# Kernel optimization log

Measured on AMD Instinct MI355X. Metric: run time of the kernel, lower is better.

Reference implementation:

```python
import jax, jax.numpy as jnp
import numpy as np
import math

N = 50000      # nodes
E = 600000     # edges
IN = 128       # in_channels
OUT = 128      # out_channels (heads * per-head)
H = 2          # heads
D = OUT // H   # per-head dim = 64
TDIM = 64      # time encoder out_channels
MSG = 64       # msg_dim
EDGE = TDIM + MSG  # edge_dim = 128


def setup_inputs() -> dict:
    key = jax.random.key(0)
    ks = jax.random.split(key, 16)
    s_in = 1.0 / math.sqrt(IN)
    s_ed = 1.0 / math.sqrt(EDGE)
    return {
        "x": jax.random.normal(ks[0], (N, IN), dtype=jnp.float32),
        "last_update": jax.random.randint(ks[1], (N,), 0, 1000000, dtype=jnp.int32),
        "edge_index": jax.random.randint(ks[2], (2, E), 0, N, dtype=jnp.int64),
        "t": jax.random.randint(ks[3], (E,), 0, 1000000, dtype=jnp.int32),
        "msg": jax.random.normal(ks[4], (E, MSG), dtype=jnp.float32),
        # TimeEncoder: cos(Linear(1 -> TDIM))
        "time_w": jax.random.normal(ks[5], (TDIM,), dtype=jnp.float32) * 0.01,
        "time_b": jax.random.normal(ks[6], (TDIM,), dtype=jnp.float32),
        # TransformerConv params (heads=2, per-head D, edge_dim=EDGE)
        "Wq": jax.random.normal(ks[7], (IN, H * D), dtype=jnp.float32) * s_in,
        "bq": jnp.zeros((H * D,), dtype=jnp.float32),
        "Wk": jax.random.normal(ks[8], (IN, H * D), dtype=jnp.float32) * s_in,
        "bk": jnp.zeros((H * D,), dtype=jnp.float32),
        "Wv": jax.random.normal(ks[9], (IN, H * D), dtype=jnp.float32) * s_in,
        "bv": jnp.zeros((H * D,), dtype=jnp.float32),
        "We": jax.random.normal(ks[10], (EDGE, H * D), dtype=jnp.float32) * s_ed,  # lin_edge, no bias
        "Wskip": jax.random.normal(ks[11], (IN, H * D), dtype=jnp.float32) * s_in,
        "bskip": jnp.zeros((H * D,), dtype=jnp.float32),
    }


def reference(x, last_update, edge_index, t, msg,
              time_w, time_b, Wq, bq, Wk, bk, Wv, bv, We, Wskip, bskip):
    src = edge_index[0]
    dst = edge_index[1]

    # rel_t = last_update[src] - t ; time encoding cos(w * rel_t + b)
    rel_t = (last_update[src] - t).astype(x.dtype)                 # [E]
    rel_t_enc = jnp.cos(rel_t[:, None] * time_w + time_b)          # [E, TDIM]
    edge_attr = jnp.concatenate([rel_t_enc, msg], axis=-1)         # [E, EDGE]

    n = x.shape[0]
    # Node projections, then per-edge gather (PyG: i = dst, j = src)
    q = (x @ Wq + bq).reshape(n, H, D)[dst]                        # [E, H, D]
    k = (x @ Wk + bk).reshape(n, H, D)[src]                        # [E, H, D]
    v = (x @ Wv + bv).reshape(n, H, D)[src]                        # [E, H, D]
    e = (edge_attr @ We).reshape(-1, H, D)                         # [E, H, D]

    k = k + e
    alpha = jnp.sum(q * k, axis=-1) / math.sqrt(D)                 # [E, H]

    # segment softmax over edges sharing the same destination node
    amax = jax.ops.segment_max(alpha, dst, num_segments=n)         # [N, H]
    ex = jnp.exp(alpha - amax[dst])                                # [E, H]
    denom = jax.ops.segment_sum(ex, dst, num_segments=n)           # [N, H]
    attn = ex / (denom[dst] + 1e-16)                               # [E, H]

    out_e = (v + e) * attn[..., None]                              # [E, H, D]
    out = jax.ops.segment_sum(out_e, dst, num_segments=n)          # [N, H, D]
    out = out.reshape(n, H * D)

    # root/skip connection (root_weight=True, beta=False)
    return out + (x @ Wskip + bskip)
```

## Files before the change

### kernel.cpp

```cpp
#include <hip/hip_runtime.h>
#include <hip/hip_bf16.h>

typedef __hip_bfloat16 bf16;
typedef __attribute__((ext_vector_type(8))) short bfrag;
typedef __attribute__((ext_vector_type(4))) float ffrag;

#define CDIM 128
#define TDIMC 64
#define MSGD 64
#define INV2PI 0.15915494309189535f
#define WCONV_BLOCKS 320

__device__ __forceinline__ unsigned short f2bf(float f) {
    union { __hip_bfloat16 h; unsigned short u; } cv;
    cv.h = __float2bfloat16(f);
    return cv.u;
}

__device__ __forceinline__ float fcos_rev(float xr) {
    float fr, c;
    asm("v_fract_f32 %0, %1" : "=v"(fr) : "v"(xr));
    asm("v_cos_f32 %0, %1" : "=v"(c) : "v"(fr));
    return c;
}

__global__ __launch_bounds__(256)
void prep_kernel(const int* __restrict__ ei, int E, int* __restrict__ count,
                 const float* __restrict__ Wq, const float* __restrict__ Wk,
                 const float* __restrict__ Wv, const float* __restrict__ Ws,
                 const float* __restrict__ We,
                 short* __restrict__ Wt, short* __restrict__ Wet) {
    int b = blockIdx.x;
    if (b < WCONV_BLOCKS) {
        int idx = b * 256 + threadIdx.x;
        if (idx >= 5 * 16384) return;
        int mat = idx >> 14;
        int r = idx & 16383;
        int n = r >> 7, kk = r & 127;
        const float* W = (mat == 0) ? Wq : (mat == 1) ? Wk : (mat == 2) ? Wv : (mat == 3) ? Ws : We;
        short bv = (short)f2bf(W[kk * 128 + n]);
        if (mat < 4) Wt[(size_t)mat * 16384 + n * 128 + kk] = bv;
        else         Wet[n * 128 + kk] = bv;
    } else {
        int e = (b - WCONV_BLOCKS) * 256 + threadIdx.x;
        int probe = (e < E) ? ei[2 * e + 1] : 0;
        int is32 = (__ballot(probe != 0) != 0ULL);
        if (e < E) {
            int d = is32 ? ei[E + e] : ei[2 * (E + e)];
            atomicAdd(&count[d], 1);
        }
    }
}

__global__ __launch_bounds__(1024)
void scan1_kernel(const int* __restrict__ count, int N,
                  int* __restrict__ cur, int* __restrict__ bsum) {
    __shared__ int wsum[16];
    __shared__ int woff[16];
    int t = threadIdx.x;
    int lane = t & 63, wv = t >> 6;
    int i = blockIdx.x * 1024 + t;
    int v = (i < N) ? count[i] : 0;
    int incl = v;
#pragma unroll
    for (int off = 1; off < 64; off <<= 1) {
        int n = __shfl_up(incl, off, 64);
        if (lane >= off) incl += n;
    }
    if (lane == 63) wsum[wv] = incl;
    __syncthreads();
    if (wv == 0) {
        int ws = (lane < 16) ? wsum[lane] : 0;
        int wi = ws;
#pragma unroll
        for (int off = 1; off < 16; off <<= 1) {
            int n = __shfl_up(wi, off, 64);
            if (lane >= off) wi += n;
        }
        if (lane < 16) woff[lane] = wi - ws;
        if (lane == 15) bsum[blockIdx.x] = wi;
    }
    __syncthreads();
    if (i < N) cur[i] = woff[wv] + incl - v;
}

__global__ void scan2_kernel(int* __restrict__ bsum, int nb) {
    int lane = threadIdx.x;
    int carry = 0;
    for (int base = 0; base < nb; base += 64) {
        int i = base + lane;
        int v = (i < nb) ? bsum[i] : 0;
        int incl = v;
#pragma unroll
        for (int off = 1; off < 64; off <<= 1) {
            int n = __shfl_up(incl, off, 64);
            if (lane >= off) incl += n;
        }
        if (i < nb) bsum[i] = carry + incl - v;
        carry += __shfl(incl, 63, 64);
    }
}

__global__ __launch_bounds__(256)
void sp_kernel(const float* __restrict__ x, const short* __restrict__ Wt,
               const float* __restrict__ bq, const float* __restrict__ bk,
               const float* __restrict__ bv, const float* __restrict__ bs,
               float* __restrict__ q, short* __restrict__ kvs,
               float* __restrict__ out, int N, int PB,
               const int* __restrict__ ei, int E,
               const int* __restrict__ tarr, const int* __restrict__ last_update,
               int* __restrict__ cur, const int* __restrict__ bsum,
               int4* __restrict__ ed_s) {
    __shared__ __attribute__((aligned(16))) short sx[64][136];
    int tid = threadIdx.x;
    if (blockIdx.x >= PB) {
        int e = (blockIdx.x - PB) * 256 + tid;
        int probe = (e < E) ? ei[2 * e + 1] : 0;
        int is32 = (__ballot(probe != 0) != 0ULL);
        if (e >= E) return;
        int s = is32 ? ei[e] : ei[2 * e];
        int d = is32 ? ei[E + e] : ei[2 * (E + e)];
        int pos = atomicAdd(&cur[d], 1) + bsum[d >> 10];
        float rt = (float)(last_update[s] - tarr[e]);
        ed_s[pos] = make_int4(s, d, e, __float_as_int(rt));
        return;
    }
    int n0 = blockIdx.x * 64;
    const float4* x4 = (const float4*)x;
    for (int i = tid; i < 64 * 32; i += 256) {
        int nl = i >> 5, c4 = i & 31;
        int n = n0 + nl;
        float4 f = (n < N) ? x4[(size_t)n * 32 + c4] : make_float4(0.f, 0.f, 0.f, 0.f);
        unsigned int lo = ((unsigned int)f2bf(f.y) << 16) | f2bf(f.x);
        unsigned int hi = ((unsigned int)f2bf(f.w) << 16) | f2bf(f.z);
        *(uint2*)&sx[nl][c4 * 4] = make_uint2(lo, hi);
    }
    __syncthreads();

    int lane = tid & 63, wv = tid >> 6;
    int n15 = lane & 15, quad = lane >> 4;
    const short* W = Wt + (size_t)wv * 16384;
    const float* bias = (wv == 0) ? bq : (wv == 1) ? bk : (wv == 2) ? bv : bs;

    ffrag acc[4][8];
#pragma unroll
    for (int r = 0; r < 4; ++r)
#pragma unroll
        for (int c = 0; c < 8; ++c)
            acc[r][c] = (ffrag){0.f, 0.f, 0.f, 0.f};

#pragma unroll
    for (int kc = 0; kc < 4; ++kc) {
        int kk = kc * 32 + quad * 8;
        bfrag a[4];
#pragma unroll
        for (int r = 0; r < 4; ++r)
            a[r] = *(const bfrag*)&sx[r * 16 + n15][kk];
#pragma unroll
        for (int c = 0; c < 8; ++c) {
            bfrag b = *(const bfrag*)&W[(c * 16 + n15) * 128 + kk];
#pragma unroll
            for (int r = 0; r < 4; ++r)
                acc[r][c] = __builtin_amdgcn_mfma_f32_16x16x32_bf16(a[r], b, acc[r][c], 0, 0, 0);
        }
    }

    if (wv == 1 || wv == 2) {
        int isv = (wv == 2) ? 2 : 0;
#pragma unroll
        for (int c = 0; c < 8; ++c) {
            int col = c * 16 + n15;
            float bval = bias[col];
            int coff = (col >> 1) * 4 + (col & 1) + isv;
#pragma unroll
            for (int r = 0; r < 4; ++r) {
#pragma unroll
                for (int g = 0; g < 4; ++g) {
                    int n = n0 + r * 16 + quad * 4 + g;
                    if (n < N) kvs[(size_t)n * 256 + coff] = (short)f2bf(acc[r][c][g] + bval);
                }
            }
        }
    } else {
        float* dstp = (wv == 0) ? q : out;
#pragma unroll
        for (int c = 0; c < 8; ++c) {
            int col = c * 16 + n15;
            float bval = bias[col];
#pragma unroll
            for (int r = 0; r < 4; ++r) {
#pragma unroll
                for (int g = 0; g < 4; ++g) {
                    int n = n0 + r * 16 + quad * 4 + g;
                    if (n < N) dstp[(size_t)n * CDIM + col] = acc[r][c][g] + bval;
                }
            }
        }
    }
}

#define LOADQ(KVA, QA, JB) do {                                                 \
    _Pragma("unroll")                                                           \
    for (int u = 0; u < 4; ++u) {                                               \
        int el = wv * 16 + (JB) * 4 + u;                                        \
        int s = s_src[el], d = s_dst[el];                                       \
        KVA[u] = kv[(size_t)s * 64 + lane];                                     \
        QA[u] = *(const float2*)&q[(size_t)d * CDIM + 2 * lane];                \
    } } while (0)

#define PROC(KVA, QA, JB) do {                                                  \
    _Pragma("unroll")                                                           \
    for (int u = 0; u < 4; ++u) {                                               \
        int el = wv * 16 + (JB) * 4 + u;                                        \
        unsigned int ep = *(const unsigned int*)&sbuf[el][2 * lane];            \
        float ex0 = __uint_as_float(ep << 16);                                  \
        float ex1 = __uint_as_float(ep & 0xffff0000u);                          \
        float kx = __uint_as_float(KVA[u].x << 16) + ex0;                       \
        float ky = __uint_as_float(KVA[u].x & 0xffff0000u) + ex1;               \
        float p = QA[u].x * kx + QA[u].y * ky;                                  \
        _Pragma("unroll")                                                       \
        for (int off = 1; off < 32; off <<= 1) p += __shfl_xor(p, off, 32);     \
        float exv = (e0 + el < E) ? __expf(p * 0.125f) : 0.f;                   \
        int d = s_dst[el];                                                      \
        if (d != cur_d) {                              \
            float* np = &num[(size_t)cur_d * CDIM + 2 * lane];                  \
            unsafeAtomicAdd(np, accx);                                          \
            unsafeAtomicAdd(np + 1, accy);                                      \
            if ((lane & 31) == 0) unsafeAtomicAdd(&den[cur_d * 2 + h], dacc);   \
            accx = 0.f; accy = 0.f; dacc = 0.f;                                 \
            cur_d = d;                                                          \
        }                                                                       \
        float vx = __uint_as_float(KVA[u].y << 16) + ex0;                       \
        float vy = __uint_as_float(KVA[u].y & 0xffff0000u) + ex1;               \
        accx = fmaf(vx, exv, accx);                                             \
        accy = fmaf(vy, exv, accy);                                             \
        dacc += exv;                                                            \
    } } while (0)

__global__ __launch_bounds__(256)
void edge_kernel(const int4* __restrict__ ed_s,
                 const float* __restrict__ msg,
                 const float* __restrict__ time_w, const float* __restrict__ time_b,
                 const short* __restrict__ Wet,
                 const float* __restrict__ q, const uint2* __restrict__ kv,
                 float* __restrict__ num, float* __restrict__ den,
                 int E) {
    __shared__ __attribute__((aligned(16))) short sbuf[64][136];
    __shared__ int s_src[64], s_dst[64];
    int tid = threadIdx.x;
    int Em1 = E - 1;

    int nwg = gridDim.x;
    int q8 = nwg >> 3, r8 = nwg & 7;
    int xcd = blockIdx.x & 7, idx8 = blockIdx.x >> 3;
    int bid = (xcd < r8 ? xcd * (q8 + 1) : r8 * (q8 + 1) + (xcd - r8) * q8) + idx8;
    int e0 = bid * 64;

    if (tid < 64) {
        int4 ed = ed_s[min(e0 + tid, Em1)];
        s_src[tid] = ed.x;
        s_dst[tid] = ed.y;
    }
    {
#pragma unroll
        for (int ii = 0; ii < 8; ++ii) {
            int i = tid + ii * 256;
            int el = i >> 5, c2 = i & 31;
            float rt = __int_as_float(ed_s[min(e0 + el, Em1)].w);
            float2 w = ((const float2*)time_w)[c2];
            float2 b = ((const float2*)time_b)[c2];
            float c0 = fcos_rev(fmaf(rt, w.x * INV2PI, b.x * INV2PI));
            float c1 = fcos_rev(fmaf(rt, w.y * INV2PI, b.y * INV2PI));
            unsigned int pk = ((unsigned int)f2bf(c1) << 16) | f2bf(c0);
            *(unsigned int*)&sbuf[el][c2 * 2] = pk;
        }
        const float4* msg4 = (const float4*)msg;
#pragma unroll
        for (int jj = 0; jj < 4; ++jj) {
            int j = tid + jj * 256;
            int el = j >> 4, f4 = j & 15;
            int p = ed_s[min(e0 + el, Em1)].z;
            float4 m = msg4[(size_t)p * 16 + f4];
            unsigned int lo = ((unsigned int)f2bf(m.y) << 16) | f2bf(m.x);
            unsigned int hi = ((unsigned int)f2bf(m.w) << 16) | f2bf(m.z);
            *(uint2*)&sbuf[el][TDIMC + f4 * 4] = make_uint2(lo, hi);
        }
    }
    __syncthreads();

    int lane = tid & 63;
    int wv = tid >> 6;
    int n15 = lane & 15, quad = lane >> 4;

    uint2 kv0[4], kv1[4], kv2[4], kv3[4];
    float2 q0[4], q1[4], q2[4], q3[4];
    LOADQ(kv0, q0, 0);
    LOADQ(kv1, q1, 1);

    ffrag acc[8];
#pragma unroll
    for (int c = 0; c < 8; ++c) acc[c] = (ffrag){0.f, 0.f, 0.f, 0.f};
#pragma unroll
    for (int kc = 0; kc < 4; ++kc) {
        int kk = kc * 32 + quad * 8;
        bfrag a = *(const bfrag*)&sbuf[wv * 16 + n15][kk];
#pragma unroll
        for (int c = 0; c < 8; ++c) {
            bfrag b = *(const bfrag*)&Wet[(c * 16 + n15) * 128 + kk];
            acc[c] = __builtin_amdgcn_mfma_f32_16x16x32_bf16(a, b, acc[c], 0, 0, 0);
        }
    }
#pragma unroll
    for (int c = 0; c < 8; ++c)
#pragma unroll
        for (int r = 0; r < 4; ++r)
            sbuf[wv * 16 + quad * 4 + r][c * 16 + n15] = (short)f2bf(acc[c][r]);

    asm volatile("s_waitcnt lgkmcnt(0)" ::: "memory");
    __builtin_amdgcn_s_barrier();
    __builtin_amdgcn_sched_barrier(0);

    int h = lane >> 5;
    float accx = 0.f, accy = 0.f, dacc = 0.f;
    int cur_d = s_dst[wv * 16];

    LOADQ(kv2, q2, 2);
    PROC(kv0, q0, 0);
    LOADQ(kv3, q3, 3);
    PROC(kv1, q1, 1);
    PROC(kv2, q2, 2);
    PROC(kv3, q3, 3);

    {
        float* np = &num[(size_t)cur_d * CDIM + 2 * lane];
        unsafeAtomicAdd(np, accx);
        unsafeAtomicAdd(np + 1, accy);
        if ((lane & 31) == 0) unsafeAtomicAdd(&den[cur_d * 2 + h], dacc);
    }
}

__global__ __launch_bounds__(256)
void norm_kernel(const float* __restrict__ num, const float* __restrict__ den,
                 float* __restrict__ out, int N) {
    int idx = blockIdx.x * 256 + threadIdx.x;
    if (idx >= N * 32) return;
    int n = idx >> 5, c4 = idx & 31;
    int h = c4 >> 4;
    float inv = 1.f / (den[n * 2 + h] + 1e-16f);
    float4 nm = ((const float4*)num)[idx];
    float4* op = (float4*)out + idx;
    float4 o = *op;
    o.x = fmaf(nm.x, inv, o.x);
    o.y = fmaf(nm.y, inv, o.y);
    o.z = fmaf(nm.z, inv, o.z);
    o.w = fmaf(nm.w, inv, o.w);
    *op = o;
}

extern "C" void kernel_launch(void* const* d_in, const int* in_sizes, int n_in,
                              void* d_out, int out_size, void* d_ws, size_t ws_size,
                              hipStream_t stream) {
    const float* x       = (const float*)d_in[0];
    const int*   last_up = (const int*)d_in[1];
    const int*   ei      = (const int*)d_in[2];
    const int*   tarr    = (const int*)d_in[3];
    const float* msg     = (const float*)d_in[4];
    const float* time_w  = (const float*)d_in[5];
    const float* time_b  = (const float*)d_in[6];
    const float* Wq = (const float*)d_in[7];  const float* bq = (const float*)d_in[8];
    const float* Wk = (const float*)d_in[9];  const float* bk = (const float*)d_in[10];
    const float* Wv = (const float*)d_in[11]; const float* bv = (const float*)d_in[12];
    const float* We = (const float*)d_in[13];
    const float* Wskip = (const float*)d_in[14]; const float* bskip = (const float*)d_in[15];
    float* out = (float*)d_out;

    int N = in_sizes[0] / CDIM;
    int E = in_sizes[3];
    int nb = (N + 1023) >> 10;

    char* ws = (char*)d_ws;
    size_t off = 0;
#define ALLOC(ptr, type, nelem) type* ptr = (type*)(ws + off); off = (off + (size_t)(nelem) * sizeof(type) + 255) & ~(size_t)255
    ALLOC(q_,    float, (size_t)N * CDIM);
    ALLOC(kvs_,  short, (size_t)N * 256);
    ALLOC(num,   float, (size_t)N * CDIM + 2 * N + N);
    float* den_ = num + (size_t)N * CDIM;
    int* count  = (int*)(den_ + 2 * N);
    ALLOC(cur,    int,  N);
    ALLOC(bsum,   int,  nb + 64);
    ALLOC(ed_s,   int4, (size_t)E);
    ALLOC(Wt,     short, 4 * 16384);
    ALLOC(Wet,    short, 16384);
#undef ALLOC

    hipMemsetAsync(num, 0, ((size_t)N * CDIM + 3 * N) * sizeof(float), stream);

    int histB = (E + 255) / 256;
    int PB = (N + 63) / 64;
    prep_kernel<<<WCONV_BLOCKS + histB, 256, 0, stream>>>(ei, E, count,
                                                          Wq, Wk, Wv, Wskip, We, Wt, Wet);
    scan1_kernel<<<nb, 1024, 0, stream>>>(count, N, cur, bsum);
    scan2_kernel<<<1, 64, 0, stream>>>(bsum, nb);
    sp_kernel<<<PB + histB, 256, 0, stream>>>(x, Wt, bq, bk, bv, bskip,
                                              q_, kvs_, out, N, PB,
                                              ei, E, tarr, last_up, cur, bsum, ed_s);
    edge_kernel<<<(E + 63) / 64, 256, 0, stream>>>(ed_s, msg, time_w, time_b, Wet,
                                                   q_, (const uint2*)kvs_, num, den_, E);
    norm_kernel<<<(N * 32 + 255) / 256, 256, 0, stream>>>(num, den_, out, N);
}
```

Measured before the change: 571.0 us.

## Swap MFMA operand roles for vectorized epilogue stores and hoist edge gathers

The node-projection and edge GEMMs now put the weights in the A operand and the activations in B. Each lane then holds four consecutive output columns of one row, so results go out as float4 and packed bf16 pairs instead of scalar shorts and floats. The edge kernel has each thread load its edge record once and cover a quarter of that edge's time-encoding and message row, replacing repeated ed_s reads. All four kv/q gather batches are also issued before the edge MFMA, to overlap more latency at the cost of registers.

```diff
diff --git a/kernel.cpp b/kernel.cpp
--- a/kernel.cpp
+++ b/kernel.cpp
@@ -105,7 +105,7 @@
 void sp_kernel(const float* __restrict__ x, const short* __restrict__ Wt,
                const float* __restrict__ bq, const float* __restrict__ bk,
                const float* __restrict__ bv, const float* __restrict__ bs,
-               float* __restrict__ q, short* __restrict__ kvs,
+               float* __restrict__ q, unsigned int* __restrict__ kvu,
                float* __restrict__ out, int N, int PB,
                const int* __restrict__ ei, int E,
                const int* __restrict__ tarr, const int* __restrict__ last_update,
@@ -142,57 +142,59 @@
     const short* W = Wt + (size_t)wv * 16384;
     const float* bias = (wv == 0) ? bq : (wv == 1) ? bk : (wv == 2) ? bv : bs;
 
-    ffrag acc[4][8];
-#pragma unroll
-    for (int r = 0; r < 4; ++r)
-#pragma unroll
-        for (int c = 0; c < 8; ++c)
-            acc[r][c] = (ffrag){0.f, 0.f, 0.f, 0.f};
+    ffrag acc[8][4];
+#pragma unroll
+    for (int oc = 0; oc < 8; ++oc)
+#pragma unroll
+        for (int nt = 0; nt < 4; ++nt)
+            acc[oc][nt] = (ffrag){0.f, 0.f, 0.f, 0.f};
 
 #pragma unroll
     for (int kc = 0; kc < 4; ++kc) {
         int kk = kc * 32 + quad * 8;
-        bfrag a[4];
-#pragma unroll
-        for (int r = 0; r < 4; ++r)
-            a[r] = *(const bfrag*)&sx[r * 16 + n15][kk];
-#pragma unroll
-        for (int c = 0; c < 8; ++c) {
-            bfrag b = *(const bfrag*)&W[(c * 16 + n15) * 128 + kk];
-#pragma unroll
-            for (int r = 0; r < 4; ++r)
-                acc[r][c] = __builtin_amdgcn_mfma_f32_16x16x32_bf16(a[r], b, acc[r][c], 0, 0, 0);
+        bfrag b[4];
+#pragma unroll
+        for (int nt = 0; nt < 4; ++nt)
+            b[nt] = *(const bfrag*)&sx[nt * 16 + n15][kk];
+#pragma unroll
+        for (int oc = 0; oc < 8; ++oc) {
+            bfrag a = *(const bfrag*)&W[(oc * 16 + n15) * 128 + kk];
+#pragma unroll
+            for (int nt = 0; nt < 4; ++nt)
+                acc[oc][nt] = __builtin_amdgcn_mfma_f32_16x16x32_bf16(a, b[nt], acc[oc][nt], 0, 0, 0);
         }
     }
 
     if (wv == 1 || wv == 2) {
-        int isv = (wv == 2) ? 2 : 0;
-#pragma unroll
-        for (int c = 0; c < 8; ++c) {
-            int col = c * 16 + n15;
-            float bval = bias[col];
-            int coff = (col >> 1) * 4 + (col & 1) + isv;
-#pragma unroll
-            for (int r = 0; r < 4; ++r) {
-#pragma unroll
-                for (int g = 0; g < 4; ++g) {
-                    int n = n0 + r * 16 + quad * 4 + g;
-                    if (n < N) kvs[(size_t)n * 256 + coff] = (short)f2bf(acc[r][c][g] + bval);
+        int iv = wv - 1;
+#pragma unroll
+        for (int oc = 0; oc < 8; ++oc) {
+            float4 b4 = *(const float4*)&bias[oc * 16 + quad * 4];
+            int d0 = oc * 16 + quad * 4 + iv;
+#pragma unroll
+            for (int nt = 0; nt < 4; ++nt) {
+                int n = n0 + nt * 16 + n15;
+                if (n < N) {
+                    ffrag a4 = acc[oc][nt];
+                    unsigned int p0 = ((unsigned int)f2bf(a4[1] + b4.y) << 16) | f2bf(a4[0] + b4.x);
+                    unsigned int p1 = ((unsigned int)f2bf(a4[3] + b4.w) << 16) | f2bf(a4[2] + b4.z);
+                    kvu[(size_t)n * 128 + d0]     = p0;
+                    kvu[(size_t)n * 128 + d0 + 2] = p1;
                 }
             }
         }
     } else {
         float* dstp = (wv == 0) ? q : out;
 #pragma unroll
-        for (int c = 0; c < 8; ++c) {
-            int col = c * 16 + n15;
-            float bval = bias[col];
-#pragma unroll
-            for (int r = 0; r < 4; ++r) {
-#pragma unroll
-                for (int g = 0; g < 4; ++g) {
-                    int n = n0 + r * 16 + quad * 4 + g;
-                    if (n < N) dstp[(size_t)n * CDIM + col] = acc[r][c][g] + bval;
+        for (int oc = 0; oc < 8; ++oc) {
+            float4 b4 = *(const float4*)&bias[oc * 16 + quad * 4];
+#pragma unroll
+            for (int nt = 0; nt < 4; ++nt) {
+                int n = n0 + nt * 16 + n15;
+                if (n < N) {
+                    ffrag a4 = acc[oc][nt];
+                    float4 o = make_float4(a4[0] + b4.x, a4[1] + b4.y, a4[2] + b4.z, a4[3] + b4.w);
+                    *(float4*)&dstp[(size_t)n * CDIM + oc * 16 + quad * 4] = o;
                 }
             }
         }
@@ -256,17 +258,14 @@
     int bid = (xcd < r8 ? xcd * (q8 + 1) : r8 * (q8 + 1) + (xcd - r8) * q8) + idx8;
     int e0 = bid * 64;
 
-    if (tid < 64) {
-        int4 ed = ed_s[min(e0 + tid, Em1)];
-        s_src[tid] = ed.x;
-        s_dst[tid] = ed.y;
-    }
     {
+        int el = tid >> 2, sub = tid & 3;
+        int4 ed = ed_s[min(e0 + el, Em1)];
+        if (sub == 0) { s_src[el] = ed.x; s_dst[el] = ed.y; }
+        float rt = __int_as_float(ed.w);
 #pragma unroll
         for (int ii = 0; ii < 8; ++ii) {
-            int i = tid + ii * 256;
-            int el = i >> 5, c2 = i & 31;
-            float rt = __int_as_float(ed_s[min(e0 + el, Em1)].w);
+            int c2 = sub * 8 + ii;
             float2 w = ((const float2*)time_w)[c2];
             float2 b = ((const float2*)time_b)[c2];
             float c0 = fcos_rev(fmaf(rt, w.x * INV2PI, b.x * INV2PI));
@@ -274,13 +273,11 @@
             unsigned int pk = ((unsigned int)f2bf(c1) << 16) | f2bf(c0);
             *(unsigned int*)&sbuf[el][c2 * 2] = pk;
         }
-        const float4* msg4 = (const float4*)msg;
+        const float4* mrow = (const float4*)msg + (size_t)ed.z * 16;
 #pragma unroll
         for (int jj = 0; jj < 4; ++jj) {
-            int j = tid + jj * 256;
-            int el = j >> 4, f4 = j & 15;
-            int p = ed_s[min(e0 + el, Em1)].z;
-            float4 m = msg4[(size_t)p * 16 + f4];
+            int f4 = sub * 4 + jj;
+            float4 m = mrow[f4];
             unsigned int lo = ((unsigned int)f2bf(m.y) << 16) | f2bf(m.x);
             unsigned int hi = ((unsigned int)f2bf(m.w) << 16) | f2bf(m.z);
             *(uint2*)&sbuf[el][TDIMC + f4 * 4] = make_uint2(lo, hi);
@@ -296,25 +293,28 @@
     float2 q0[4], q1[4], q2[4], q3[4];
     LOADQ(kv0, q0, 0);
     LOADQ(kv1, q1, 1);
+    LOADQ(kv2, q2, 2);
+    LOADQ(kv3, q3, 3);
 
     ffrag acc[8];
 #pragma unroll
-    for (int c = 0; c < 8; ++c) acc[c] = (ffrag){0.f, 0.f, 0.f, 0.f};
+    for (int oc = 0; oc < 8; ++oc) acc[oc] = (ffrag){0.f, 0.f, 0.f, 0.f};
 #pragma unroll
     for (int kc = 0; kc < 4; ++kc) {
         int kk = kc * 32 + quad * 8;
-        bfrag a = *(const bfrag*)&sbuf[wv * 16 + n15][kk];
-#pragma unroll
-        for (int c = 0; c < 8; ++c) {
-            bfrag b = *(const bfrag*)&Wet[(c * 16 + n15) * 128 + kk];
-            acc[c] = __builtin_amdgcn_mfma_f32_16x16x32_bf16(a, b, acc[c], 0, 0, 0);
-        }
-    }
-#pragma unroll
-    for (int c = 0; c < 8; ++c)
-#pragma unroll
-        for (int r = 0; r < 4; ++r)
-            sbuf[wv * 16 + quad * 4 + r][c * 16 + n15] = (short)f2bf(acc[c][r]);
+        bfrag b = *(const bfrag*)&sbuf[wv * 16 + n15][kk];
+#pragma unroll
+        for (int oc = 0; oc < 8; ++oc) {
+            bfrag a = *(const bfrag*)&Wet[(oc * 16 + n15) * 128 + kk];
+            acc[oc] = __builtin_amdgcn_mfma_f32_16x16x32_bf16(a, b, acc[oc], 0, 0, 0);
+        }
+    }
+#pragma unroll
+    for (int oc = 0; oc < 8; ++oc) {
+        unsigned int lo = ((unsigned int)f2bf(acc[oc][1]) << 16) | f2bf(acc[oc][0]);
+        unsigned int hi = ((unsigned int)f2bf(acc[oc][3]) << 16) | f2bf(acc[oc][2]);
+        *(uint2*)&sbuf[wv * 16 + n15][oc * 16 + quad * 4] = make_uint2(lo, hi);
+    }
 
     asm volatile("s_waitcnt lgkmcnt(0)" ::: "memory");
     __builtin_amdgcn_s_barrier();
@@ -324,9 +324,7 @@
     float accx = 0.f, accy = 0.f, dacc = 0.f;
     int cur_d = s_dst[wv * 16];
 
-    LOADQ(kv2, q2, 2);
     PROC(kv0, q0, 0);
-    LOADQ(kv3, q3, 3);
     PROC(kv1, q1, 1);
     PROC(kv2, q2, 2);
     PROC(kv3, q3, 3);
@@ -402,7 +400,7 @@
     scan1_kernel<<<nb, 1024, 0, stream>>>(count, N, cur, bsum);
     scan2_kernel<<<1, 64, 0, stream>>>(bsum, nb);
     sp_kernel<<<PB + histB, 256, 0, stream>>>(x, Wt, bq, bk, bv, bskip,
-                                              q_, kvs_, out, N, PB,
+                                              q_, (unsigned int*)kvs_, out, N, PB,
                                               ei, E, tarr, last_up, cur, bsum, ed_s);
     edge_kernel<<<(E + 63) / 64, 256, 0, stream>>>(ed_s, msg, time_w, time_b, Wet,
                                                    q_, (const uint2*)kvs_, num, den_, E);
```

After: 559.7 us. 1.02x faster.
